# Kernel optimization log

Hardware: AMD Instinct MI355X
Metric: run time of the kernel (lower is better)

Reference implementation:

```python
import jax, jax.numpy as jnp
import numpy as np

B, N, E = 32, 1024, 16384
IN_DIM, HID, OUT = 768, 512, 400
H, F = 2, 200          # gat heads, per-head dim (H*F == OUT)
PAIR = 2 * OUT         # 800
NEG_SLOPE = 0.2


def setup_inputs() -> dict:
    key = jax.random.key(0)
    ks = jax.random.split(key, 20)
    g = lambda k, shp, fan: jax.random.normal(k, shp, jnp.float32) * (1.0 / np.sqrt(fan))
    return {
        "patch_features": jax.random.normal(ks[0], (B, N, IN_DIM), jnp.float32),
        "edges": jax.random.randint(ks[1], (2, E), 0, N, jnp.int32),
        # patch_encoder Mlps: 768 -> 512 (GELU) -> 400
        "enc_w1": g(ks[2], (IN_DIM, HID), IN_DIM), "enc_b1": jnp.zeros((HID,), jnp.float32),
        "enc_w2": g(ks[3], (HID, OUT), HID),      "enc_b2": jnp.zeros((OUT,), jnp.float32),
        # single GATConv: 400 -> 2 heads x 200, concat
        "gat_w": g(ks[4], (OUT, H, F), OUT),
        "att_src": g(ks[5], (H, F), F), "att_dst": g(ks[6], (H, F), F),
        "gat_b": jnp.zeros((H * F,), jnp.float32),
        # predict_head Mlps: 800 -> 800 (GELU) -> 400 (GELU) -> 3
        "h_w1": g(ks[7], (PAIR, PAIR), PAIR),      "h_b1": jnp.zeros((PAIR,), jnp.float32),
        "h_w2": g(ks[8], (PAIR, PAIR // 2), PAIR), "h_b2": jnp.zeros((PAIR // 2,), jnp.float32),
        "h_w3": g(ks[9], (PAIR // 2, 3), PAIR // 2), "h_b3": jnp.zeros((3,), jnp.float32),
    }


def _forward(patch_features, edges, enc_w1, enc_b1, enc_w2, enc_b2,
             gat_w, att_src, att_dst, gat_b,
             h_w1, h_b1, h_w2, h_b2, h_w3, h_b3):
    n = patch_features.shape[1]
    # per-batch patch encoder MLP (dropout inactive at eval)
    enc = jax.nn.gelu(jnp.einsum('bni,ih->bnh', patch_features, enc_w1) + enc_b1)
    enc = jnp.einsum('bnh,ho->bno', enc, enc_w2) + enc_b2   # [B,N,400]

    src0, dst0 = edges[0], edges[1]
    # GATConv adds self-loops
    loops = jnp.arange(n, dtype=edges.dtype)
    src = jnp.concatenate([src0, loops])
    dst = jnp.concatenate([dst0, loops])

    def gat(h):                                   # h: [N,400]
        wh = jnp.einsum('no,ohf->nhf', h, gat_w)  # [N,H,F]
        a_s = jnp.sum(wh * att_src, -1)           # [N,H]
        a_d = jnp.sum(wh * att_dst, -1)
        e = a_s[src] + a_d[dst]                   # [Et,H]
        e = jnp.where(e > 0, e, NEG_SLOPE * e)    # LeakyReLU(0.2)
        m = jax.ops.segment_max(e, dst, num_segments=n)
        ee = jnp.exp(e - m[dst])
        z = jax.ops.segment_sum(ee, dst, num_segments=n)
        coef = ee / z[dst]                        # softmax over incoming edges
        out = jax.ops.segment_sum(coef[:, :, None] * wh[src], dst, num_segments=n)
        return out.reshape(n, H * F) + gat_b      # concat heads + bias

    feat = enc + jax.vmap(gat)(enc)               # residual add per batch

    # pairwise edge gather + predict head
    pair = jnp.concatenate([feat[:, src0], feat[:, dst0]], axis=-1)  # [B,E,800]
    p = jax.nn.gelu(jnp.einsum('bep,pq->beq', pair, h_w1) + h_b1)
    p = jax.nn.gelu(jnp.einsum('beq,qr->ber', p, h_w2) + h_b2)
    pred = jnp.einsum('ber,rs->bes', p, h_w3) + h_b3                 # [B,E,3]
    return feat, pred


def reference(patch_features, edges, enc_w1, enc_b1, enc_w2, enc_b2,
              gat_w, att_src, att_dst, gat_b,
              h_w1, h_b1, h_w2, h_b2, h_w3, h_b3):
    return _forward(patch_features, edges, enc_w1, enc_b1, enc_w2, enc_b2,
                    gat_w, att_src, att_dst, gat_b,
                    h_w1, h_b1, h_w2, h_b2, h_w3, h_b3)
```

## Files before the change

kernel.cpp:

```cpp
#include <hip/hip_runtime.h>
#include <hip/hip_bf16.h>

typedef unsigned short u16;
typedef __attribute__((ext_vector_type(8))) short bf16x8;
typedef __attribute__((ext_vector_type(4))) float f32x4;

#define B_   32
#define N_   1024
#define E_   16384
#define ET_  17408
#define IN_DIM 768
#define HID  512
#define OUT_ 400
#define PAIR_ 800
#define UVW_ 1600
#define FEAT_ELEMS 13107200
#define MAXD 128

__device__ __forceinline__ float u2f(u16 u) {
    union { unsigned int i; float f; } v; v.i = ((unsigned int)u) << 16; return v.f;
}
__device__ __forceinline__ u16 f2u(float f) {
    __hip_bfloat16 h = __float2bfloat16(f);
    return *(u16*)&h;
}
__device__ __forceinline__ unsigned int pack2(float a, float b) {
    return (unsigned int)f2u(a) | ((unsigned int)f2u(b) << 16);
}

__device__ __forceinline__ float gelu_f(float x) {
    const float c = 0.7978845608028654f;
    float u = c * (x + 0.044715f * x * x * x);
    float t = 2.0f / (1.0f + __expf(-2.0f * u)) - 1.0f;
    return 0.5f * x * (1.0f + t);
}

__device__ __forceinline__ void load_lds16(const void* g, void* l) {
    __builtin_amdgcn_global_load_lds(
        (const __attribute__((address_space(1))) void*)g,
        (__attribute__((address_space(3))) void*)l, 16, 0, 0);
}

__global__ void wt_k(const float* __restrict__ W, u16* __restrict__ Wt,
                     int K, int N)
{
    int i = blockIdx.x * 256 + threadIdx.x;
    if (i >= N * K) return;
    int n = i / K, k = i - n * K;
    Wt[i] = f2u(W[(size_t)k * N + n]);
}

__global__ void wtuv_k(const float* __restrict__ W, u16* __restrict__ Wt)
{
    int i = blockIdx.x * 256 + threadIdx.x;
    if (i >= UVW_ * OUT_) return;
    int n = i / OUT_, k = i - n * OUT_;
    int row = (n >= PAIR_) ? OUT_ + k : k;
    int col = (n >= PAIR_) ? n - PAIR_ : n;
    Wt[i] = f2u(W[(size_t)row * PAIR_ + col]);
}

__global__ void f2b_k(const float* __restrict__ X, u16* __restrict__ Y, int n8)
{
    int i = blockIdx.x * 256 + threadIdx.x;
    if (i >= n8) return;
    const float4* p = (const float4*)X + (size_t)i * 2;
    float4 a = p[0], b = p[1];
    uint4 o;
    o.x = pack2(a.x, a.y); o.y = pack2(a.z, a.w);
    o.z = pack2(b.x, b.y); o.w = pack2(b.z, b.w);
    ((uint4*)Y)[i] = o;
}

template<int ASRC, bool DO_GELU, bool HAS_BIAS, bool OUT_F32, bool FUSE_H3, bool WIDE>
__global__ __launch_bounds__(WIDE ? 512 : 256, 2)
void mfma_gemm_k(const float* __restrict__ Af, const u16* __restrict__ Ab,
                 const u16* __restrict__ Wt, const float* __restrict__ bias,
                 u16* __restrict__ Cb, float* __restrict__ Cf,
                 int M, int N, int K,
                 const u16* __restrict__ zbuf,
                 const float* __restrict__ w3p, float* __restrict__ partp)
{
    static_assert(!WIDE || ASRC == 1, "wide path requires bf16 async staging");
    constexpr int BM  = WIDE ? 256 : 128;
    constexpr int BN  = WIDE ? 256 : 128;
    constexpr int NWV = WIDE ? 8 : 4;
    constexpr int UN  = WIDE ? 8 : 4;
    constexpr int WNS = WIDE ? 128 : 64;

    __shared__ __align__(16) u16 As[2][BM * 64];
    __shared__ __align__(16) u16 Bs[2][BN * 64];
    const int tid  = threadIdx.x;
    const int gx   = gridDim.x;
    const int nwg  = gx * gridDim.y;
    const int orig = blockIdx.y * gx + blockIdx.x;
    const int qc   = nwg >> 3, rc = nwg & 7;
    const int xcd  = orig & 7, lid = orig >> 3;
    const int wg   = ((xcd < rc) ? xcd * (qc + 1) : rc * (qc + 1) + (xcd - rc) * qc) + lid;
    const int bnIdx= wg % gx;
    const int bm   = (wg / gx) * BM;
    const int bn   = bnIdx * BN;
    const int wave = tid >> 6;
    const int lane = tid & 63;
    const int wm   = (wave >> 1) * 64;
    const int wn   = (wave & 1) * WNS;
    const int lm   = lane & 15;
    const int lq   = lane >> 4;
    const int lb   = lm & 7;
    const int l8 = lane >> 3;
    const int cl = (lane & 7) ^ l8;

    size_t arow[4]; size_t brow[4]; bool bok[4];
    #pragma unroll
    for (int c4 = 0; c4 < 4; ++c4) {
        int rt = wave * 32 + c4 * 8 + l8;
        if (ASRC == 1) arow[c4] = (size_t)(bm + rt) * K;
        int n = bn + rt;
        bok[c4] = (n < N);
        brow[c4] = (size_t)(n < N ? n : 0) * K;
    }
    const int vrow = tid >> 1, vhalf = tid & 1;

    f32x4 acc[4][UN] = {};
    const int NT = (K + 63) >> 6;

    if (ASRC == 1) {
        auto stage = [&](int buf, int k0) {
            int kk = k0 + cl * 8;
            #pragma unroll
            for (int c4 = 0; c4 < 4; ++c4) {
                const u16* ga = (kk < K) ? Ab + arow[c4] + kk : zbuf;
                load_lds16(ga, (char*)As[buf] + (wave * 32 + c4 * 8) * 128);
            }
            #pragma unroll
            for (int c4 = 0; c4 < 4; ++c4) {
                const u16* gb = (bok[c4] && kk < K) ? Wt + brow[c4] + kk : zbuf;
                load_lds16(gb, (char*)Bs[buf] + (wave * 32 + c4 * 8) * 128);
            }
        };
        stage(0, 0);
        int cur = 0;
        for (int it = 0; it < NT; ++it) {
            const bool last = (it == NT - 1);
            if (!last) stage(cur ^ 1, (it + 1) * 64);
            if (!last) asm volatile("s_waitcnt vmcnt(8)" ::: "memory");
            else       asm volatile("s_waitcnt vmcnt(0)" ::: "memory");
            __builtin_amdgcn_s_barrier();
            const char* Abase = (const char*)As[cur];
            const char* Bbase = (const char*)Bs[cur];
            #pragma unroll
            for (int kh = 0; kh < 2; ++kh) {
                bf16x8 af[4], bfr[UN];
                #pragma unroll
                for (int t = 0; t < 4; ++t)
                    af[t] = *(const bf16x8*)(Abase +
                            (wm + t * 16 + lm) * 128 + (((kh * 4 + lq) ^ lb) * 16));
                #pragma unroll
                for (int u = 0; u < UN; ++u)
                    bfr[u] = *(const bf16x8*)(Bbase +
                            (wn + u * 16 + lm) * 128 + (((kh * 4 + lq) ^ lb) * 16));
                #pragma unroll
                for (int t = 0; t < 4; ++t)
                    #pragma unroll
                    for (int u = 0; u < UN; ++u)
                        acc[t][u] = __builtin_amdgcn_mfma_f32_16x16x32_bf16(
                            af[t], bfr[u], acc[t][u], 0, 0, 0);
            }
            asm volatile("" ::: "memory");
            __builtin_amdgcn_s_barrier();
            cur ^= 1;
        }
    } else {
        for (int k0 = 0; k0 < K; k0 += 64) {
            #pragma unroll
            for (int c = 0; c < 4; ++c) {
                int c_log = vhalf * 4 + c;
                int kk = k0 + c_log * 8;
                uint4 wv = make_uint4(0, 0, 0, 0);
                if (kk < K) {
                    const float* p = Af + (size_t)(bm + vrow) * K + kk;
                    float4 v0 = *(const float4*)p;
                    float4 v1 = *(const float4*)(p + 4);
                    wv.x = pack2(v0.x, v0.y); wv.y = pack2(v0.z, v0.w);
                    wv.z = pack2(v1.x, v1.y); wv.w = pack2(v1.z, v1.w);
                }
                int pc = c_log ^ (vrow & 7);
                *(uint4*)((char*)As[0] + vrow * 128 + pc * 16) = wv;
            }
            {
                int kk = k0 + cl * 8;
                #pragma unroll
                for (int c4 = 0; c4 < 4; ++c4) {
                    const u16* gb = (bok[c4] && kk < K) ? Wt + brow[c4] + kk : zbuf;
                    load_lds16(gb, (char*)Bs[0] + (wave * 32 + c4 * 8) * 128);
                }
            }
            __syncthreads();
            #pragma unroll
            for (int kh = 0; kh < 2; ++kh) {
                bf16x8 af[4], bfr[UN];
                #pragma unroll
                for (int t = 0; t < 4; ++t)
                    af[t] = *(const bf16x8*)((const char*)As[0] +
                            (wm + t * 16 + lm) * 128 + (((kh * 4 + lq) ^ lb) * 16));
                #pragma unroll
                for (int u = 0; u < UN; ++u)
                    bfr[u] = *(const bf16x8*)((const char*)Bs[0] +
                            (wn + u * 16 + lm) * 128 + (((kh * 4 + lq) ^ lb) * 16));
                #pragma unroll
                for (int t = 0; t < 4; ++t)
                    #pragma unroll
                    for (int u = 0; u < UN; ++u)
                        acc[t][u] = __builtin_amdgcn_mfma_f32_16x16x32_bf16(
                            af[t], bfr[u], acc[t][u], 0, 0, 0);
            }
            __syncthreads();
        }
    }

    if (FUSE_H3) {
        float w3c[UN][3]; float bvv[UN];
        #pragma unroll
        for (int u = 0; u < UN; ++u) {
            int col = bn + wn + u * 16 + lm;
            bool ok = (col < N);
            bvv[u]    = ok ? bias[col] : 0.f;
            w3c[u][0] = ok ? w3p[col * 3 + 0] : 0.f;
            w3c[u][1] = ok ? w3p[col * 3 + 1] : 0.f;
            w3c[u][2] = ok ? w3p[col * 3 + 2] : 0.f;
        }
        float* red = (float*)As;
        #pragma unroll
        for (int t = 0; t < 4; ++t) {
            #pragma unroll
            for (int r = 0; r < 4; ++r) {
                float s0 = 0.f, s1 = 0.f, s2 = 0.f;
                #pragma unroll
                for (int u = 0; u < UN; ++u) {
                    float v = gelu_f(acc[t][u][r] + bvv[u]);
                    s0 += v * w3c[u][0];
                    s1 += v * w3c[u][1];
                    s2 += v * w3c[u][2];
                }
                #pragma unroll
                for (int off = 8; off; off >>= 1) {
                    s0 += __shfl_xor(s0, off);
                    s1 += __shfl_xor(s1, off);
                    s2 += __shfl_xor(s2, off);
                }
                if (lm == 0) {
                    int lr = t * 16 + lq * 4 + r;
                    float* d = red + (wave * 64 + lr) * 3;
                    d[0] = s0; d[1] = s1; d[2] = s2;
                }
            }
        }
        __syncthreads();
        if ((wave & 1) == 0) {
            int lr = lane;
            int rowg = bm + wm + lr;
            float* a = red + ((wave + 0) * 64 + lr) * 3;
            float* b = red + ((wave + 1) * 64 + lr) * 3;
            float* d = partp + ((size_t)bnIdx * M + rowg) * 3;
            d[0] = a[0] + b[0];
            d[1] = a[1] + b[1];
            d[2] = a[2] + b[2];
        }
        return;
    }

    #pragma unroll
    for (int u = 0; u < UN; ++u) {
        int col = bn + wn + u * 16 + lm;
        if (col >= N) continue;
        float bv = HAS_BIAS ? bias[col] : 0.f;
        #pragma unroll
        for (int t = 0; t < 4; ++t) {
            #pragma unroll
            for (int r = 0; r < 4; ++r) {
                int rowg = bm + wm + t * 16 + lq * 4 + r;
                float v = acc[t][u][r] + bv;
                if (DO_GELU) v = gelu_f(v);
                if (OUT_F32) {
                    Cf[(size_t)rowg * N + col] = v;
                    if (Cb) Cb[(size_t)rowg * N + col] = f2u(v);
                } else {
                    Cb[(size_t)rowg * N + col] = f2u(v);
                }
            }
        }
    }
}

__global__ __launch_bounds__(256)
void red3_k(const float* __restrict__ part, const float* __restrict__ b3,
            float* __restrict__ out, int row_base, int Mr, int ns)
{
    int r = blockIdx.x * 256 + threadIdx.x;
    if (r >= Mr) return;
    float s0 = b3[0], s1 = b3[1], s2 = b3[2];
    for (int s = 0; s < ns; ++s) {
        const float* p = part + ((size_t)s * Mr + r) * 3;
        s0 += p[0]; s1 += p[1]; s2 += p[2];
    }
    float* d = out + (size_t)FEAT_ELEMS + (size_t)(row_base + r) * 3;
    d[0] = s0; d[1] = s1; d[2] = s2;
}

__global__ __launch_bounds__(256)
void pair_fuse_k(const u16* __restrict__ UV, const float* __restrict__ b1,
                 const int* __restrict__ src0, const int* __restrict__ dst0,
                 u16* __restrict__ p1, int b0, int nrows)
{
    unsigned idx = blockIdx.x * 256u + threadIdx.x;
    unsigned total = (unsigned)nrows * 100u;
    if (idx >= total) return;
    unsigned r  = (unsigned)(((unsigned long long)idx * 1374389535ull) >> 37);
    unsigned c8 = idx - r * 100u;
    int e = r & (E_ - 1);
    int gs, gd;
    if (b0 >= 0) {
        int b = b0 + (int)(r >> 14);
        gs = (b << 10) + src0[e];
        gd = (b << 10) + dst0[e];
    } else {
        gs = src0[e]; gd = dst0[e];
    }
    uint4 qu = *(const uint4*)(UV + (size_t)gs * UVW_ + c8 * 8);
    uint4 qv = *(const uint4*)(UV + (size_t)gd * UVW_ + PAIR_ + c8 * 8);
    float4 bva = *(const float4*)(b1 + c8 * 8);
    float4 bvb = *(const float4*)(b1 + c8 * 8 + 4);
    float bb[8] = {bva.x, bva.y, bva.z, bva.w, bvb.x, bvb.y, bvb.z, bvb.w};
    unsigned int uu[4] = {qu.x, qu.y, qu.z, qu.w};
    unsigned int vv[4] = {qv.x, qv.y, qv.z, qv.w};
    uint4 o; unsigned int* op = (unsigned int*)&o;
    #pragma unroll
    for (int q = 0; q < 4; ++q) {
        float a0 = u2f((u16)(uu[q] & 0xffff)) + u2f((u16)(vv[q] & 0xffff)) + bb[2*q];
        float a1 = u2f((u16)(uu[q] >> 16))    + u2f((u16)(vv[q] >> 16))    + bb[2*q+1];
        op[q] = pack2(gelu_f(a0), gelu_f(a1));
    }
    *(uint4*)(p1 + (size_t)r * PAIR_ + c8 * 8) = o;
}

__global__ __launch_bounds__(256)
void scores_k(const u16* __restrict__ wh, const float* __restrict__ att_s,
              const float* __restrict__ att_d, float* __restrict__ a_s,
              float* __restrict__ a_d)
{
    int n = blockIdx.x * 4 + (threadIdx.x >> 6);
    int lane = threadIdx.x & 63;
    const u16* row = wh + (size_t)n * OUT_;
    float as0 = 0, as1 = 0, ad0 = 0, ad1 = 0;
    for (int f = lane; f < OUT_; f += 64) {
        float v = u2f(row[f]);
        float s = att_s[f];
        float d = att_d[f];
        if (f < 200) { as0 += v * s; ad0 += v * d; }
        else         { as1 += v * s; ad1 += v * d; }
    }
    for (int off = 32; off; off >>= 1) {
        as0 += __shfl_xor(as0, off); as1 += __shfl_xor(as1, off);
        ad0 += __shfl_xor(ad0, off); ad1 += __shfl_xor(ad1, off);
    }
    if (lane == 0) {
        a_s[(size_t)n * 2 + 0] = as0; a_s[(size_t)n * 2 + 1] = as1;
        a_d[(size_t)n * 2 + 0] = ad0; a_d[(size_t)n * 2 + 1] = ad1;
    }
}

__global__ void csr_count_k(const int* __restrict__ edges, int* __restrict__ deg)
{
    int et = blockIdx.x * blockDim.x + threadIdx.x;
    if (et >= ET_) return;
    int dst = (et < E_) ? edges[E_ + et] : (et - E_);
    atomicAdd(&deg[dst], 1);
}

__global__ __launch_bounds__(1024)
void csr_scan_k(const int* __restrict__ deg, int* __restrict__ row_ptr,
                int* __restrict__ cnt)
{
    __shared__ int s[1024];
    int t = threadIdx.x;
    int d = deg[t];
    s[t] = d;
    __syncthreads();
    for (int off = 1; off < 1024; off <<= 1) {
        int v = (t >= off) ? s[t - off] : 0;
        __syncthreads();
        s[t] += v;
        __syncthreads();
    }
    row_ptr[t] = s[t] - d;
    cnt[t] = s[t] - d;
    if (t == 1023) row_ptr[1024] = s[t];
}

__global__ void csr_fill_k(const int* __restrict__ edges, int* __restrict__ cnt,
                           int* __restrict__ col_src)
{
    int et = blockIdx.x * blockDim.x + threadIdx.x;
    if (et >= ET_) return;
    int src, dst;
    if (et < E_) { src = edges[et]; dst = edges[E_ + et]; }
    else         { src = et - E_;  dst = src; }
    int pos = atomicAdd(&cnt[dst], 1);
    col_src[pos] = src;
}

__global__ __launch_bounds__(256)
void gat_k(const u16* __restrict__ wh,
           const float* __restrict__ a_s, const float* __restrict__ a_d,
           const int* __restrict__ row_ptr, const int* __restrict__ col_src,
           const float* __restrict__ gat_b, float* __restrict__ feat,
           u16* __restrict__ featb16)
{
    int gn = blockIdx.x;
    int b = gn >> 10, n = gn & 1023;
    int tid = threadIdx.x;
    __shared__ float s_ee[2][MAXD];
    __shared__ int   s_src[MAXD];
    __shared__ float s_misc[6];
    __shared__ float s_part[4][50][9];
    int start = row_ptr[n];
    int deg = row_ptr[n + 1] - start;

    if (tid < 64) {
        int lane = tid;
        float ad0 = a_d[(size_t)gn * 2 + 0];
        float ad1 = a_d[(size_t)gn * 2 + 1];
        float m0 = -1e30f, m1 = -1e30f;
        for (int j = lane; j < deg; j += 64) {
            int gs = (b << 10) + col_src[start + j];
            float e0 = a_s[(size_t)gs * 2 + 0] + ad0; e0 = (e0 > 0.f) ? e0 : 0.2f * e0;
            float e1 = a_s[(size_t)gs * 2 + 1] + ad1; e1 = (e1 > 0.f) ? e1 : 0.2f * e1;
            if (j < MAXD) { s_ee[0][j] = e0; s_ee[1][j] = e1; s_src[j] = gs; }
            m0 = fmaxf(m0, e0); m1 = fmaxf(m1, e1);
        }
        for (int off = 32; off; off >>= 1) {
            m0 = fmaxf(m0, __shfl_xor(m0, off));
            m1 = fmaxf(m1, __shfl_xor(m1, off));
        }
        float z0 = 0.f, z1 = 0.f;
        for (int j = lane; j < deg; j += 64) {
            float e0, e1;
            if (j < MAXD) { e0 = s_ee[0][j]; e1 = s_ee[1][j]; }
            else {
                int gs = (b << 10) + col_src[start + j];
                e0 = a_s[(size_t)gs * 2 + 0] + ad0; e0 = (e0 > 0.f) ? e0 : 0.2f * e0;
                e1 = a_s[(size_t)gs * 2 + 1] + ad1; e1 = (e1 > 0.f) ? e1 : 0.2f * e1;
            }
            float t0 = __expf(e0 - m0), t1 = __expf(e1 - m1);
            if (j < MAXD) { s_ee[0][j] = t0; s_ee[1][j] = t1; }
            z0 += t0; z1 += t1;
        }
        for (int off = 32; off; off >>= 1) {
            z0 += __shfl_xor(z0, off);
            z1 += __shfl_xor(z1, off);
        }
        if (lane == 0) {
            s_misc[0] = m0; s_misc[1] = m1;
            s_misc[2] = (z0 > 0.f) ? 1.f / z0 : 0.f;
            s_misc[3] = (z1 > 0.f) ? 1.f / z1 : 0.f;
            s_misc[4] = ad0; s_misc[5] = ad1;
        }
    }
    __syncthreads();

    int wv = tid >> 6, ln = tid & 63;
    if (ln < 50) {
        int h = (ln >= 25);
        float m = s_misc[h], ad = s_misc[4 + h];
        float acc[8] = {};
        for (int j = wv; j < deg; j += 4) {
            float w; int gs;
            if (j < MAXD) { w = s_ee[h][j]; gs = s_src[j]; }
            else {
                gs = (b << 10) + col_src[start + j];
                float e = a_s[(size_t)gs * 2 + h] + ad;
                e = (e > 0.f) ? e : 0.2f * e;
                w = __expf(e - m);
            }
            uint4 q = *(const uint4*)(wh + (size_t)gs * OUT_ + ln * 8);
            acc[0] += w * u2f((u16)(q.x & 0xffff));
            acc[1] += w * u2f((u16)(q.x >> 16));
            acc[2] += w * u2f((u16)(q.y & 0xffff));
            acc[3] += w * u2f((u16)(q.y >> 16));
            acc[4] += w * u2f((u16)(q.z & 0xffff));
            acc[5] += w * u2f((u16)(q.z >> 16));
            acc[6] += w * u2f((u16)(q.w & 0xffff));
            acc[7] += w * u2f((u16)(q.w >> 16));
        }
        #pragma unroll
        for (int k = 0; k < 8; ++k) s_part[wv][ln][k] = acc[k];
    }
    __syncthreads();
    if (tid < 50) {
        int h = (tid >= 25);
        float iz = s_misc[2 + h];
        size_t base = (size_t)gn * OUT_ + tid * 8;
        float4 f0 = *(const float4*)(feat + base);
        float4 f1 = *(const float4*)(feat + base + 4);
        float fv[8] = { f0.x, f0.y, f0.z, f0.w, f1.x, f1.y, f1.z, f1.w };
        float o[8];
        #pragma unroll
        for (int k = 0; k < 8; ++k) {
            float s = s_part[0][tid][k] + s_part[1][tid][k] +
                      s_part[2][tid][k] + s_part[3][tid][k];
            o[k] = fv[k] + s * iz + gat_b[tid * 8 + k];
        }
        *(float4*)(feat + base)     = make_float4(o[0], o[1], o[2], o[3]);
        *(float4*)(feat + base + 4) = make_float4(o[4], o[5], o[6], o[7]);
        if (featb16) {
            uint4 bq;
            bq.x = pack2(o[0], o[1]); bq.y = pack2(o[2], o[3]);
            bq.z = pack2(o[4], o[5]); bq.w = pack2(o[6], o[7]);
            *(uint4*)(featb16 + base) = bq;
        }
    }
}

__global__ __launch_bounds__(256)
void head3_k(const u16* __restrict__ p2, const float* __restrict__ w3,
             const float* __restrict__ b3, float* __restrict__ out,
             int row_base, int nrows)
{
    int wv = threadIdx.x >> 6, lane = threadIdx.x & 63;
    float w3r[24];
    if (lane < 50) {
        #pragma unroll
        for (int q = 0; q < 6; ++q) {
            float4 v = *(const float4*)(w3 + lane * 24 + q * 4);
            w3r[q * 4 + 0] = v.x; w3r[q * 4 + 1] = v.y;
            w3r[q * 4 + 2] = v.z; w3r[q * 4 + 3] = v.w;
        }
    }
    int e0 = blockIdx.x * 16 + wv * 4;
    for (int ei = 0; ei < 4; ++ei) {
        int e = e0 + ei;
        if (e >= nrows) break;
        float s0 = 0, s1 = 0, s2 = 0;
        if (lane < 50) {
            uint4 q = *(const uint4*)(p2 + (size_t)e * OUT_ + lane * 8);
            float f[8];
            f[0] = u2f((u16)(q.x & 0xffff)); f[1] = u2f((u16)(q.x >> 16));
            f[2] = u2f((u16)(q.y & 0xffff)); f[3] = u2f((u16)(q.y >> 16));
            f[4] = u2f((u16)(q.z & 0xffff)); f[5] = u2f((u16)(q.z >> 16));
            f[6] = u2f((u16)(q.w & 0xffff)); f[7] = u2f((u16)(q.w >> 16));
            #pragma unroll
            for (int k = 0; k < 8; ++k) {
                s0 += f[k] * w3r[k * 3 + 0];
                s1 += f[k] * w3r[k * 3 + 1];
                s2 += f[k] * w3r[k * 3 + 2];
            }
        }
        for (int off = 32; off; off >>= 1) {
            s0 += __shfl_xor(s0, off);
            s1 += __shfl_xor(s1, off);
            s2 += __shfl_xor(s2, off);
        }
        if (lane == 0) {
            size_t o = (size_t)FEAT_ELEMS + (size_t)(row_base + e) * 3;
            out[o + 0] = s0 + b3[0];
            out[o + 1] = s1 + b3[1];
            out[o + 2] = s2 + b3[2];
        }
    }
}

extern "C" void kernel_launch(void* const* d_in, const int* in_sizes, int n_in,
                              void* d_out, int out_size, void* d_ws, size_t ws_size,
                              hipStream_t stream)
{
    const float* patch  = (const float*)d_in[0];
    const int*   edges  = (const int*)d_in[1];
    const float* enc_w1 = (const float*)d_in[2];
    const float* enc_b1 = (const float*)d_in[3];
    const float* enc_w2 = (const float*)d_in[4];
    const float* enc_b2 = (const float*)d_in[5];
    const float* gat_w  = (const float*)d_in[6];
    const float* att_s  = (const float*)d_in[7];
    const float* att_d  = (const float*)d_in[8];
    const float* gat_b  = (const float*)d_in[9];
    const float* h_w1   = (const float*)d_in[10];
    const float* h_b1   = (const float*)d_in[11];
    const float* h_w2   = (const float*)d_in[12];
    const float* h_b2   = (const float*)d_in[13];
    const float* h_w3   = (const float*)d_in[14];
    const float* h_b3   = (const float*)d_in[15];
    float* out  = (float*)d_out;
    float* feat = out;
    char*  ws   = (char*)d_ws;

    const int* src0 = edges;
    const int* dst0 = edges + E_;

    const size_t R0 = 33554432ull, TAIL = 4194304ull;
    const size_t UVSZ = 104857600ull;
    const size_t P1SZ = 26214400ull;
    int CB = 0;
    if      (ws_size >= R0 + UVSZ + TAIL + 4 * P1SZ) CB = 4;
    else if (ws_size >= R0 + UVSZ + TAIL + 2 * P1SZ) CB = 2;
    const bool big = (CB >= 2);

    u16 *enc1, *whb, *p1, *p2, *featb16, *uv, *w1t, *w2t, *gwt, *uvwt, *hw2t;
    u16 *patchb16, *encb16;
    float *a_s, *a_d, *part; int *deg;
    if (big) {
        enc1    = (u16*)ws;
        featb16 = (u16*)ws;
        part    = (float*)ws;
        whb     = (u16*)(ws + R0);
        uv      = (u16*)(ws + R0);
        encb16  = (u16*)(ws + R0 + 26214400ull);
        p1      = (u16*)(ws + R0 + UVSZ);
        patchb16= (u16*)(ws + R0 + UVSZ);
        p2      = nullptr;
        size_t tb = (ws_size - TAIL) & ~(size_t)255;
        w1t  = (u16*)(ws + tb);
        w2t  = (u16*)(ws + tb + 786432);
        gwt  = (u16*)(ws + tb + 1196032);
        uvwt = (u16*)(ws + tb + 1516032);
        hw2t = (u16*)(ws + tb + 2796032);
        a_s  = (float*)(ws + tb + 3436032);
        a_d  = (float*)(ws + tb + 3698176);
        deg  = (int*)(ws + tb + 3960320);
    } else {
        enc1    = (u16*)ws;
        whb     = (u16*)ws;
        p1      = (u16*)ws;
        featb16 = nullptr;
        patchb16= nullptr;
        encb16  = nullptr;
        part    = nullptr;
        p2      = (u16*)(ws + 26214400);
        uv      = (u16*)(ws + 39321600);
        w1t  = (u16*)(ws + 42598400);
        w2t  = (u16*)(ws + 43384832);
        gwt  = (u16*)(ws + 43794432);
        uvwt = (u16*)(ws + 44114432);
        hw2t = (u16*)(ws + 45394432);
        a_s  = (float*)(ws + 46034432);
        a_d  = (float*)(ws + 46296576);
        deg  = (int*)(ws + 46558720);
    }
    int* row_ptr = deg + 1024;
    int* cnt     = row_ptr + 1032;
    int* col_src = cnt + 1024;
    u16* zbuf = (u16*)(col_src + 17408);

    hipMemsetAsync(zbuf, 0, 256, stream);

    wt_k<<<(HID * IN_DIM + 255) / 256, 256, 0, stream>>>(enc_w1, w1t, IN_DIM, HID);
    wt_k<<<(OUT_ * HID + 255) / 256, 256, 0, stream>>>(enc_w2, w2t, HID, OUT_);
    wt_k<<<(OUT_ * OUT_ + 255) / 256, 256, 0, stream>>>(gat_w, gwt, OUT_, OUT_);
    wtuv_k<<<(UVW_ * OUT_ + 255) / 256, 256, 0, stream>>>(h_w1, uvwt);
    wt_k<<<(OUT_ * PAIR_ + 255) / 256, 256, 0, stream>>>(h_w2, hw2t, PAIR_, OUT_);

    hipMemsetAsync(deg, 0, 1024 * sizeof(int), stream);
    csr_count_k<<<(ET_ + 255) / 256, 256, 0, stream>>>(edges, deg);
    csr_scan_k<<<1, 1024, 0, stream>>>(deg, row_ptr, cnt);
    csr_fill_k<<<(ET_ + 255) / 256, 256, 0, stream>>>(edges, cnt, col_src);

    if (big) {
        f2b_k<<<(B_ * N_ * IN_DIM / 8 + 255) / 256, 256, 0, stream>>>(
            patch, patchb16, B_ * N_ * IN_DIM / 8);
        mfma_gemm_k<1, true, true, false, false, true><<<dim3(2, (B_ * N_) / 256), 512, 0, stream>>>(
            nullptr, patchb16, w1t, enc_b1, enc1, nullptr, B_ * N_, HID, IN_DIM, zbuf,
            nullptr, nullptr);
        mfma_gemm_k<1, false, true, true, false, true><<<dim3(2, (B_ * N_) / 256), 512, 0, stream>>>(
            nullptr, enc1, w2t, enc_b2, encb16, feat, B_ * N_, OUT_, HID, zbuf,
            nullptr, nullptr);
        mfma_gemm_k<1, false, false, false, false, true><<<dim3(2, (B_ * N_) / 256), 512, 0, stream>>>(
            nullptr, encb16, gwt, nullptr, whb, nullptr, B_ * N_, OUT_, OUT_, zbuf,
            nullptr, nullptr);
    } else {
        mfma_gemm_k<0, true, true, false, false, false><<<dim3(HID / 128, (B_ * N_) / 128), 256, 0, stream>>>(
            patch, nullptr, w1t, enc_b1, enc1, nullptr, B_ * N_, HID, IN_DIM, zbuf,
            nullptr, nullptr);
        mfma_gemm_k<1, false, true, true, false, false><<<dim3((OUT_ + 127) / 128, (B_ * N_) / 128), 256, 0, stream>>>(
            nullptr, enc1, w2t, enc_b2, nullptr, feat, B_ * N_, OUT_, HID, zbuf,
            nullptr, nullptr);
        mfma_gemm_k<0, false, false, false, false, false><<<dim3((OUT_ + 127) / 128, (B_ * N_) / 128), 256, 0, stream>>>(
            feat, nullptr, gwt, nullptr, whb, nullptr, B_ * N_, OUT_, OUT_, zbuf,
            nullptr, nullptr);
    }

    scores_k<<<(B_ * N_) / 4, 256, 0, stream>>>(whb, att_s, att_d, a_s, a_d);
    gat_k<<<B_ * N_, 256, 0, stream>>>(whb, a_s, a_d, row_ptr, col_src,
                                       gat_b, feat, featb16);

    if (big) {
        mfma_gemm_k<1, false, false, false, false, true><<<dim3((UVW_ + 255) / 256, (B_ * N_) / 256), 512, 0, stream>>>(
            nullptr, featb16, uvwt, nullptr, uv, nullptr, B_ * N_, UVW_, OUT_, zbuf,
            nullptr, nullptr);
        for (int b0 = 0; b0 < B_; b0 += CB) {
            int Mr = CB * E_;
            pair_fuse_k<<<(Mr * 100 + 255) / 256, 256, 0, stream>>>(
                uv, h_b1, src0, dst0, p1, b0, Mr);
            mfma_gemm_k<1, true, true, false, true, true><<<dim3((OUT_ + 255) / 256, Mr / 256), 512, 0, stream>>>(
                nullptr, p1, hw2t, h_b2, nullptr, nullptr, Mr, OUT_, PAIR_, zbuf,
                h_w3, part);
            red3_k<<<(Mr + 255) / 256, 256, 0, stream>>>(part, h_b3, out, b0 * E_, Mr,
                                                         (OUT_ + 255) / 256);
        }
    } else {
        for (int b = 0; b < B_; ++b) {
            const float* featb = feat + (size_t)b * N_ * OUT_;
            mfma_gemm_k<0, false, false, false, false, false><<<dim3((UVW_ + 127) / 128, N_ / 128), 256, 0, stream>>>(
                featb, nullptr, uvwt, nullptr, uv, nullptr, N_, UVW_, OUT_, zbuf,
                nullptr, nullptr);
            pair_fuse_k<<<(E_ * 100 + 255) / 256, 256, 0, stream>>>(
                uv, h_b1, src0, dst0, p1, -1, E_);
            mfma_gemm_k<1, true, true, false, false, false><<<dim3((OUT_ + 127) / 128, E_ / 128), 256, 0, stream>>>(
                nullptr, p1, hw2t, h_b2, p2, nullptr, E_, OUT_, PAIR_, zbuf,
                nullptr, nullptr);
            head3_k<<<(E_ + 15) / 16, 256, 0, stream>>>(p2, h_w3, h_b3, out,
                                                        b * E_, E_);
        }
    }
}
```

Measured before the change: 1.502 ms.

## Add 128x512 GEMM tile shape for predict-head layer 2 to cover full N

Adds a third tile shape (BM=128, BN=512, BK=32, 8 waves in a 2x4 layout) to the MFMA GEMM. It is used for the fused h_w2+h_w3 predict-head GEMM so one block covers all 400 output columns. Previously N=400 was split across two 256-wide blocks, which padded the second block heavily and made the A tile load twice. The partial-sum buffer and the red3 reduction now handle a single column block. The trade-offs are a shorter K step, which means more barriers per tile, a different LDS swizzle, and 112 of the 512 columns still padded.

```diff
diff --git a/kernel.cpp b/kernel.cpp
--- a/kernel.cpp
+++ b/kernel.cpp
@@ -72,8 +72,8 @@
     ((uint4*)Y)[i] = o;
 }
 
-template<int ASRC, bool DO_GELU, bool HAS_BIAS, bool OUT_F32, bool FUSE_H3, bool WIDE>
-__global__ __launch_bounds__(WIDE ? 512 : 256, 2)
+template<int ASRC, bool DO_GELU, bool HAS_BIAS, bool OUT_F32, bool FUSE_H3, int SHAPE>
+__global__ __launch_bounds__(SHAPE >= 1 ? 512 : 256, 2)
 void mfma_gemm_k(const float* __restrict__ Af, const u16* __restrict__ Ab,
                  const u16* __restrict__ Wt, const float* __restrict__ bias,
                  u16* __restrict__ Cb, float* __restrict__ Cf,
@@ -81,15 +81,17 @@
                  const u16* __restrict__ zbuf,
                  const float* __restrict__ w3p, float* __restrict__ partp)
 {
-    static_assert(!WIDE || ASRC == 1, "wide path requires bf16 async staging");
-    constexpr int BM  = WIDE ? 256 : 128;
-    constexpr int BN  = WIDE ? 256 : 128;
-    constexpr int NWV = WIDE ? 8 : 4;
-    constexpr int UN  = WIDE ? 8 : 4;
-    constexpr int WNS = WIDE ? 128 : 64;
-
-    __shared__ __align__(16) u16 As[2][BM * 64];
-    __shared__ __align__(16) u16 Bs[2][BN * 64];
+    static_assert(SHAPE == 0 || ASRC == 1, "wide shapes require bf16 async staging");
+    constexpr int BM  = (SHAPE == 2) ? 128 : (SHAPE == 1 ? 256 : 128);
+    constexpr int BN  = (SHAPE == 2) ? 512 : (SHAPE == 1 ? 256 : 128);
+    constexpr int NWV = (SHAPE >= 1) ? 8 : 4;
+    constexpr int UN  = (SHAPE >= 1) ? 8 : 4;
+    constexpr int BKT = (SHAPE == 2) ? 32 : 64;
+    constexpr int KH  = (SHAPE == 2) ? 1 : 2;
+    constexpr int CW  = (SHAPE == 2) ? 4 : 2;
+
+    __shared__ __align__(16) u16 As[2][BM * BKT];
+    __shared__ __align__(16) u16 Bs[2][BN * BKT];
     const int tid  = threadIdx.x;
     const int gx   = gridDim.x;
     const int nwg  = gx * gridDim.y;
@@ -102,63 +104,101 @@
     const int bn   = bnIdx * BN;
     const int wave = tid >> 6;
     const int lane = tid & 63;
-    const int wm   = (wave >> 1) * 64;
-    const int wn   = (wave & 1) * WNS;
+    const int wm   = (SHAPE == 2) ? (wave >> 2) * 64 : (wave >> 1) * 64;
+    const int wn   = (SHAPE == 2) ? (wave & 3) * 128
+                   : (SHAPE == 1) ? (wave & 1) * 128 : (wave & 1) * 64;
     const int lm   = lane & 15;
     const int lq   = lane >> 4;
     const int lb   = lm & 7;
     const int l8 = lane >> 3;
     const int cl = (lane & 7) ^ l8;
+    const int l4 = lane >> 2;
+    const int ck = lane & 3;
+    const int cl2 = ck ^ ((l4 >> 1) & 3);
 
     size_t arow[4]; size_t brow[4]; bool bok[4];
-    #pragma unroll
-    for (int c4 = 0; c4 < 4; ++c4) {
-        int rt = wave * 32 + c4 * 8 + l8;
-        if (ASRC == 1) arow[c4] = (size_t)(bm + rt) * K;
-        int n = bn + rt;
-        bok[c4] = (n < N);
-        brow[c4] = (size_t)(n < N ? n : 0) * K;
+    size_t arowS = 0;
+    if (SHAPE == 2) {
+        arowS = (size_t)(bm + wave * 16 + l4) * K;
+        #pragma unroll
+        for (int c4 = 0; c4 < 4; ++c4) {
+            int n = bn + wave * 64 + c4 * 16 + l4;
+            bok[c4] = (n < N);
+            brow[c4] = (size_t)(n < N ? n : 0) * K;
+        }
+    } else {
+        #pragma unroll
+        for (int c4 = 0; c4 < 4; ++c4) {
+            int rt = wave * 32 + c4 * 8 + l8;
+            if (ASRC == 1) arow[c4] = (size_t)(bm + rt) * K;
+            int n = bn + rt;
+            bok[c4] = (n < N);
+            brow[c4] = (size_t)(n < N ? n : 0) * K;
+        }
     }
     const int vrow = tid >> 1, vhalf = tid & 1;
 
     f32x4 acc[4][UN] = {};
-    const int NT = (K + 63) >> 6;
+    const int NT = (K + BKT - 1) / BKT;
 
     if (ASRC == 1) {
         auto stage = [&](int buf, int k0) {
-            int kk = k0 + cl * 8;
-            #pragma unroll
-            for (int c4 = 0; c4 < 4; ++c4) {
-                const u16* ga = (kk < K) ? Ab + arow[c4] + kk : zbuf;
-                load_lds16(ga, (char*)As[buf] + (wave * 32 + c4 * 8) * 128);
-            }
-            #pragma unroll
-            for (int c4 = 0; c4 < 4; ++c4) {
-                const u16* gb = (bok[c4] && kk < K) ? Wt + brow[c4] + kk : zbuf;
-                load_lds16(gb, (char*)Bs[buf] + (wave * 32 + c4 * 8) * 128);
+            if (SHAPE == 2) {
+                int kk = k0 + cl2 * 8;
+                const u16* ga = (kk < K) ? Ab + arowS + kk : zbuf;
+                load_lds16(ga, (char*)As[buf] + wave * 16 * 64);
+                #pragma unroll
+                for (int c4 = 0; c4 < 4; ++c4) {
+                    const u16* gb = (bok[c4] && kk < K) ? Wt + brow[c4] + kk : zbuf;
+                    load_lds16(gb, (char*)Bs[buf] + (wave * 64 + c4 * 16) * 64);
+                }
+            } else {
+                int kk = k0 + cl * 8;
+                #pragma unroll
+                for (int c4 = 0; c4 < 4; ++c4) {
+                    const u16* ga = (kk < K) ? Ab + arow[c4] + kk : zbuf;
+                    load_lds16(ga, (char*)As[buf] + (wave * 32 + c4 * 8) * 128);
+                }
+                #pragma unroll
+                for (int c4 = 0; c4 < 4; ++c4) {
+                    const u16* gb = (bok[c4] && kk < K) ? Wt + brow[c4] + kk : zbuf;
+                    load_lds16(gb, (char*)Bs[buf] + (wave * 32 + c4 * 8) * 128);
+                }
             }
         };
         stage(0, 0);
         int cur = 0;
         for (int it = 0; it < NT; ++it) {
             const bool last = (it == NT - 1);
-            if (!last) stage(cur ^ 1, (it + 1) * 64);
-            if (!last) asm volatile("s_waitcnt vmcnt(8)" ::: "memory");
-            else       asm volatile("s_waitcnt vmcnt(0)" ::: "memory");
+            if (!last) stage(cur ^ 1, (it + 1) * BKT);
+            if (!last) {
+                if (SHAPE == 2) asm volatile("s_waitcnt vmcnt(5)" ::: "memory");
+                else            asm volatile("s_waitcnt vmcnt(8)" ::: "memory");
+            } else {
+                asm volatile("s_waitcnt vmcnt(0)" ::: "memory");
+            }
             __builtin_amdgcn_s_barrier();
             const char* Abase = (const char*)As[cur];
             const char* Bbase = (const char*)Bs[cur];
             #pragma unroll
-            for (int kh = 0; kh < 2; ++kh) {
+            for (int kh = 0; kh < KH; ++kh) {
                 bf16x8 af[4], bfr[UN];
                 #pragma unroll
-                for (int t = 0; t < 4; ++t)
-                    af[t] = *(const bf16x8*)(Abase +
-                            (wm + t * 16 + lm) * 128 + (((kh * 4 + lq) ^ lb) * 16));
-                #pragma unroll
-                for (int u = 0; u < UN; ++u)
-                    bfr[u] = *(const bf16x8*)(Bbase +
-                            (wn + u * 16 + lm) * 128 + (((kh * 4 + lq) ^ lb) * 16));
+                for (int t = 0; t < 4; ++t) {
+                    int row = wm + t * 16 + lm;
+                    int off = (SHAPE == 2)
+                        ? row * 64 + ((lq ^ ((row >> 1) & 3)) * 16)
+                        : row * 128 + (((kh * 4 + lq) ^ lb) * 16);
+                    af[t] = *(const bf16x8*)(Abase + off);
+                }
+                #pragma unroll
+                for (int u = 0; u < UN; ++u) {
+                    int row = wn + u * 16 + lm;
+                    int off = (SHAPE == 2)
+                        ? row * 64 + ((lq ^ ((row >> 1) & 3)) * 16)
+                        : row * 128 + (((kh * 4 + lq) ^ lb) * 16);
+                    bfr[u] = *(const bf16x8*)(Bbase + off);
+                }
                 #pragma unroll
                 for (int t = 0; t < 4; ++t)
                     #pragma unroll
@@ -256,15 +296,17 @@
             }
         }
         __syncthreads();
-        if ((wave & 1) == 0) {
+        if ((wave & (CW - 1)) == 0) {
             int lr = lane;
             int rowg = bm + wm + lr;
-            float* a = red + ((wave + 0) * 64 + lr) * 3;
-            float* b = red + ((wave + 1) * 64 + lr) * 3;
+            float s0 = 0.f, s1 = 0.f, s2 = 0.f;
+            #pragma unroll
+            for (int w = 0; w < CW; ++w) {
+                float* a = red + ((wave + w) * 64 + lr) * 3;
+                s0 += a[0]; s1 += a[1]; s2 += a[2];
+            }
             float* d = partp + ((size_t)bnIdx * M + rowg) * 3;
-            d[0] = a[0] + b[0];
-            d[1] = a[1] + b[1];
-            d[2] = a[2] + b[2];
+            d[0] = s0; d[1] = s1; d[2] = s2;
         }
         return;
     }
@@ -666,23 +708,23 @@
     if (big) {
         f2b_k<<<(B_ * N_ * IN_DIM / 8 + 255) / 256, 256, 0, stream>>>(
             patch, patchb16, B_ * N_ * IN_DIM / 8);
-        mfma_gemm_k<1, true, true, false, false, true><<<dim3(2, (B_ * N_) / 256), 512, 0, stream>>>(
+        mfma_gemm_k<1, true, true, false, false, 1><<<dim3(2, (B_ * N_) / 256), 512, 0, stream>>>(
             nullptr, patchb16, w1t, enc_b1, enc1, nullptr, B_ * N_, HID, IN_DIM, zbuf,
             nullptr, nullptr);
-        mfma_gemm_k<1, false, true, true, false, true><<<dim3(2, (B_ * N_) / 256), 512, 0, stream>>>(
+        mfma_gemm_k<1, false, true, true, false, 1><<<dim3(2, (B_ * N_) / 256), 512, 0, stream>>>(
             nullptr, enc1, w2t, enc_b2, encb16, feat, B_ * N_, OUT_, HID, zbuf,
             nullptr, nullptr);
-        mfma_gemm_k<1, false, false, false, false, true><<<dim3(2, (B_ * N_) / 256), 512, 0, stream>>>(
+        mfma_gemm_k<1, false, false, false, false, 1><<<dim3(2, (B_ * N_) / 256), 512, 0, stream>>>(
             nullptr, encb16, gwt, nullptr, whb, nullptr, B_ * N_, OUT_, OUT_, zbuf,
             nullptr, nullptr);
     } else {
-        mfma_gemm_k<0, true, true, false, false, false><<<dim3(HID / 128, (B_ * N_) / 128), 256, 0, stream>>>(
+        mfma_gemm_k<0, true, true, false, false, 0><<<dim3(HID / 128, (B_ * N_) / 128), 256, 0, stream>>>(
             patch, nullptr, w1t, enc_b1, enc1, nullptr, B_ * N_, HID, IN_DIM, zbuf,
             nullptr, nullptr);
-        mfma_gemm_k<1, false, true, true, false, false><<<dim3((OUT_ + 127) / 128, (B_ * N_) / 128), 256, 0, stream>>>(
+        mfma_gemm_k<1, false, true, true, false, 0><<<dim3((OUT_ + 127) / 128, (B_ * N_) / 128), 256, 0, stream>>>(
             nullptr, enc1, w2t, enc_b2, nullptr, feat, B_ * N_, OUT_, HID, zbuf,
             nullptr, nullptr);
-        mfma_gemm_k<0, false, false, false, false, false><<<dim3((OUT_ + 127) / 128, (B_ * N_) / 128), 256, 0, stream>>>(
+        mfma_gemm_k<0, false, false, false, false, 0><<<dim3((OUT_ + 127) / 128, (B_ * N_) / 128), 256, 0, stream>>>(
             feat, nullptr, gwt, nullptr, whb, nullptr, B_ * N_, OUT_, OUT_, zbuf,
             nullptr, nullptr);
     }
@@ -692,28 +734,27 @@
                                        gat_b, feat, featb16);
 
     if (big) {
-        mfma_gemm_k<1, false, false, false, false, true><<<dim3((UVW_ + 255) / 256, (B_ * N_) / 256), 512, 0, stream>>>(
+        mfma_gemm_k<1, false, false, false, false, 1><<<dim3((UVW_ + 255) / 256, (B_ * N_) / 256), 512, 0, stream>>>(
             nullptr, featb16, uvwt, nullptr, uv, nullptr, B_ * N_, UVW_, OUT_, zbuf,
             nullptr, nullptr);
         for (int b0 = 0; b0 < B_; b0 += CB) {
             int Mr = CB * E_;
             pair_fuse_k<<<(Mr * 100 + 255) / 256, 256, 0, stream>>>(
                 uv, h_b1, src0, dst0, p1, b0, Mr);
-            mfma_gemm_k<1, true, true, false, true, true><<<dim3((OUT_ + 255) / 256, Mr / 256), 512, 0, stream>>>(
+            mfma_gemm_k<1, true, true, false, true, 2><<<dim3(1, Mr / 128), 512, 0, stream>>>(
                 nullptr, p1, hw2t, h_b2, nullptr, nullptr, Mr, OUT_, PAIR_, zbuf,
                 h_w3, part);
-            red3_k<<<(Mr + 255) / 256, 256, 0, stream>>>(part, h_b3, out, b0 * E_, Mr,
-                                                         (OUT_ + 255) / 256);
+            red3_k<<<(Mr + 255) / 256, 256, 0, stream>>>(part, h_b3, out, b0 * E_, Mr, 1);
         }
     } else {
         for (int b = 0; b < B_; ++b) {
             const float* featb = feat + (size_t)b * N_ * OUT_;
-            mfma_gemm_k<0, false, false, false, false, false><<<dim3((UVW_ + 127) / 128, N_ / 128), 256, 0, stream>>>(
+            mfma_gemm_k<0, false, false, false, false, 0><<<dim3((UVW_ + 127) / 128, N_ / 128), 256, 0, stream>>>(
                 featb, nullptr, uvwt, nullptr, uv, nullptr, N_, UVW_, OUT_, zbuf,
                 nullptr, nullptr);
             pair_fuse_k<<<(E_ * 100 + 255) / 256, 256, 0, stream>>>(
                 uv, h_b1, src0, dst0, p1, -1, E_);
-            mfma_gemm_k<1, true, true, false, false, false><<<dim3((OUT_ + 127) / 128, E_ / 128), 256, 0, stream>>>(
+            mfma_gemm_k<1, true, true, false, false, 0><<<dim3((OUT_ + 127) / 128, E_ / 128), 256, 0, stream>>>(
                 nullptr, p1, hw2t, h_b2, p2, nullptr, E_, OUT_, PAIR_, zbuf,
                 nullptr, nullptr);
             head3_k<<<(E_ + 15) / 16, 256, 0, stream>>>(p2, h_w3, h_b3, out,
```

Result: slower. 1.641 ms (+9.2%).

## Fuse pair gather, bias and GELU into head GEMM A-tile staging

Applied to the files above, without the earlier changes.

The separate pair_fuse kernel and its p1 intermediate go away. The second head GEMM now gathers the u and v rows by src/dst edge index directly during A-tile staging, adds h_b1, applies GELU and writes the bf16 tile to LDS. This removes the write and reread of the large p1 buffer and the per-chunk launch loop, so all batches run in one launch. In exchange the A operand uses synchronous register loads plus ALU work inside the pipelined loop instead of async LDS loads, which may weaken load/compute overlap, and the GELU is recomputed for each of the two N-tiles.

```diff
diff --git a/kernel.cpp b/kernel.cpp
--- a/kernel.cpp
+++ b/kernel.cpp
@@ -72,21 +72,22 @@
     ((uint4*)Y)[i] = o;
 }
 
-template<int ASRC, bool DO_GELU, bool HAS_BIAS, bool OUT_F32, bool FUSE_H3, bool WIDE>
-__global__ __launch_bounds__(WIDE ? 512 : 256, 2)
+template<int ASRC, bool DO_GELU, bool HAS_BIAS, bool OUT_F32, bool FUSE_H3, int SHAPE>
+__global__ __launch_bounds__(SHAPE >= 1 ? 512 : 256, 2)
 void mfma_gemm_k(const float* __restrict__ Af, const u16* __restrict__ Ab,
                  const u16* __restrict__ Wt, const float* __restrict__ bias,
                  u16* __restrict__ Cb, float* __restrict__ Cf,
                  int M, int N, int K,
                  const u16* __restrict__ zbuf,
-                 const float* __restrict__ w3p, float* __restrict__ partp)
-{
-    static_assert(!WIDE || ASRC == 1, "wide path requires bf16 async staging");
-    constexpr int BM  = WIDE ? 256 : 128;
-    constexpr int BN  = WIDE ? 256 : 128;
-    constexpr int NWV = WIDE ? 8 : 4;
-    constexpr int UN  = WIDE ? 8 : 4;
-    constexpr int WNS = WIDE ? 128 : 64;
+                 const float* __restrict__ w3p, float* __restrict__ partp,
+                 const int* __restrict__ src0p, const int* __restrict__ dst0p,
+                 int b0)
+{
+    static_assert(SHAPE == 0 || ASRC >= 1, "wide shapes need bf16/gather staging");
+    constexpr int BM  = (SHAPE == 1) ? 256 : 128;
+    constexpr int BN  = (SHAPE == 1) ? 256 : 128;
+    constexpr int UN  = (SHAPE == 1) ? 8 : 4;
+    constexpr int CW  = 2;
 
     __shared__ __align__(16) u16 As[2][BM * 64];
     __shared__ __align__(16) u16 Bs[2][BN * 64];
@@ -103,7 +104,7 @@
     const int wave = tid >> 6;
     const int lane = tid & 63;
     const int wm   = (wave >> 1) * 64;
-    const int wn   = (wave & 1) * WNS;
+    const int wn   = (SHAPE == 1) ? (wave & 1) * 128 : (wave & 1) * 64;
     const int lm   = lane & 15;
     const int lq   = lane >> 4;
     const int lb   = lm & 7;
@@ -119,23 +120,77 @@
         bok[c4] = (n < N);
         brow[c4] = (size_t)(n < N ? n : 0) * K;
     }
+    int gsv[4], gdv[4];
+    if (ASRC == 2) {
+        #pragma unroll
+        for (int c = 0; c < 4; ++c) {
+            int gr = bm + wave * 32 + c * 8 + (lane >> 3);
+            int e  = gr & (E_ - 1);
+            int b  = b0 + (gr >> 14);
+            gsv[c] = (b << 10) + src0p[e];
+            gdv[c] = (b << 10) + dst0p[e];
+        }
+    }
     const int vrow = tid >> 1, vhalf = tid & 1;
 
     f32x4 acc[4][UN] = {};
     const int NT = (K + 63) >> 6;
 
-    if (ASRC == 1) {
+    if (ASRC >= 1) {
         auto stage = [&](int buf, int k0) {
-            int kk = k0 + cl * 8;
-            #pragma unroll
-            for (int c4 = 0; c4 < 4; ++c4) {
-                const u16* ga = (kk < K) ? Ab + arow[c4] + kk : zbuf;
-                load_lds16(ga, (char*)As[buf] + (wave * 32 + c4 * 8) * 128);
-            }
-            #pragma unroll
-            for (int c4 = 0; c4 < 4; ++c4) {
-                const u16* gb = (bok[c4] && kk < K) ? Wt + brow[c4] + kk : zbuf;
-                load_lds16(gb, (char*)Bs[buf] + (wave * 32 + c4 * 8) * 128);
+            if (ASRC == 2) {
+                int kk  = k0 + (lane & 7) * 8;
+                int kkb = k0 + cl * 8;
+                bool okk = (kk < PAIR_);
+                uint4 qu[4], qv[4];
+                float4 bA = make_float4(0, 0, 0, 0), bB = bA;
+                if (okk) {
+                    bA = *(const float4*)(Af + kk);
+                    bB = *(const float4*)(Af + kk + 4);
+                    #pragma unroll
+                    for (int c = 0; c < 4; ++c) {
+                        qu[c] = *(const uint4*)(Ab + (size_t)gsv[c] * UVW_ + kk);
+                        qv[c] = *(const uint4*)(Ab + (size_t)gdv[c] * UVW_ + PAIR_ + kk);
+                    }
+                }
+                #pragma unroll
+                for (int c4 = 0; c4 < 4; ++c4) {
+                    const u16* gb = (bok[c4] && kkb < K) ? Wt + brow[c4] + kkb : zbuf;
+                    load_lds16(gb, (char*)Bs[buf] + (wave * 32 + c4 * 8) * 128);
+                }
+                float bb[8] = {bA.x, bA.y, bA.z, bA.w, bB.x, bB.y, bB.z, bB.w};
+                #pragma unroll
+                for (int c = 0; c < 4; ++c) {
+                    int r = wave * 32 + c * 8 + (lane >> 3);
+                    uint4 wv = make_uint4(0, 0, 0, 0);
+                    if (okk) {
+                        unsigned uu[4] = {qu[c].x, qu[c].y, qu[c].z, qu[c].w};
+                        unsigned vv[4] = {qv[c].x, qv[c].y, qv[c].z, qv[c].w};
+                        unsigned* op = (unsigned*)&wv;
+                        #pragma unroll
+                        for (int q = 0; q < 4; ++q) {
+                            float a0 = u2f((u16)(uu[q] & 0xffff)) +
+                                       u2f((u16)(vv[q] & 0xffff)) + bb[2 * q];
+                            float a1 = u2f((u16)(uu[q] >> 16)) +
+                                       u2f((u16)(vv[q] >> 16)) + bb[2 * q + 1];
+                            op[q] = pack2(gelu_f(a0), gelu_f(a1));
+                        }
+                    }
+                    int pc = (lane & 7) ^ (r & 7);
+                    *(uint4*)((char*)As[buf] + r * 128 + pc * 16) = wv;
+                }
+            } else {
+                int kk = k0 + cl * 8;
+                #pragma unroll
+                for (int c4 = 0; c4 < 4; ++c4) {
+                    const u16* ga = (kk < K) ? Ab + arow[c4] + kk : zbuf;
+                    load_lds16(ga, (char*)As[buf] + (wave * 32 + c4 * 8) * 128);
+                }
+                #pragma unroll
+                for (int c4 = 0; c4 < 4; ++c4) {
+                    const u16* gb = (bok[c4] && kk < K) ? Wt + brow[c4] + kk : zbuf;
+                    load_lds16(gb, (char*)Bs[buf] + (wave * 32 + c4 * 8) * 128);
+                }
             }
         };
         stage(0, 0);
@@ -143,8 +198,12 @@
         for (int it = 0; it < NT; ++it) {
             const bool last = (it == NT - 1);
             if (!last) stage(cur ^ 1, (it + 1) * 64);
-            if (!last) asm volatile("s_waitcnt vmcnt(8)" ::: "memory");
-            else       asm volatile("s_waitcnt vmcnt(0)" ::: "memory");
+            if (!last) {
+                if (ASRC == 2) asm volatile("s_waitcnt vmcnt(4) lgkmcnt(0)" ::: "memory");
+                else           asm volatile("s_waitcnt vmcnt(8)" ::: "memory");
+            } else {
+                asm volatile("s_waitcnt vmcnt(0) lgkmcnt(0)" ::: "memory");
+            }
             __builtin_amdgcn_s_barrier();
             const char* Abase = (const char*)As[cur];
             const char* Bbase = (const char*)Bs[cur];
@@ -256,15 +315,17 @@
             }
         }
         __syncthreads();
-        if ((wave & 1) == 0) {
+        if ((wave & (CW - 1)) == 0) {
             int lr = lane;
             int rowg = bm + wm + lr;
-            float* a = red + ((wave + 0) * 64 + lr) * 3;
-            float* b = red + ((wave + 1) * 64 + lr) * 3;
+            float s0 = 0.f, s1 = 0.f, s2 = 0.f;
+            #pragma unroll
+            for (int w = 0; w < CW; ++w) {
+                float* a = red + ((wave + w) * 64 + lr) * 3;
+                s0 += a[0]; s1 += a[1]; s2 += a[2];
+            }
             float* d = partp + ((size_t)bnIdx * M + rowg) * 3;
-            d[0] = a[0] + b[0];
-            d[1] = a[1] + b[1];
-            d[2] = a[2] + b[2];
+            d[0] = s0; d[1] = s1; d[2] = s2;
         }
         return;
     }
@@ -599,10 +660,7 @@
     const size_t R0 = 33554432ull, TAIL = 4194304ull;
     const size_t UVSZ = 104857600ull;
     const size_t P1SZ = 26214400ull;
-    int CB = 0;
-    if      (ws_size >= R0 + UVSZ + TAIL + 4 * P1SZ) CB = 4;
-    else if (ws_size >= R0 + UVSZ + TAIL + 2 * P1SZ) CB = 2;
-    const bool big = (CB >= 2);
+    const bool big = (ws_size >= R0 + UVSZ + TAIL + 2 * P1SZ);
 
     u16 *enc1, *whb, *p1, *p2, *featb16, *uv, *w1t, *w2t, *gwt, *uvwt, *hw2t;
     u16 *patchb16, *encb16;
@@ -614,8 +672,8 @@
         whb     = (u16*)(ws + R0);
         uv      = (u16*)(ws + R0);
         encb16  = (u16*)(ws + R0 + 26214400ull);
-        p1      = (u16*)(ws + R0 + UVSZ);
         patchb16= (u16*)(ws + R0 + UVSZ);
+        p1      = nullptr;
         p2      = nullptr;
         size_t tb = (ws_size - TAIL) & ~(size_t)255;
         w1t  = (u16*)(ws + tb);
@@ -666,25 +724,25 @@
     if (big) {
         f2b_k<<<(B_ * N_ * IN_DIM / 8 + 255) / 256, 256, 0, stream>>>(
             patch, patchb16, B_ * N_ * IN_DIM / 8);
-        mfma_gemm_k<1, true, true, false, false, true><<<dim3(2, (B_ * N_) / 256), 512, 0, stream>>>(
+        mfma_gemm_k<1, true, true, false, false, 1><<<dim3(2, (B_ * N_) / 256), 512, 0, stream>>>(
             nullptr, patchb16, w1t, enc_b1, enc1, nullptr, B_ * N_, HID, IN_DIM, zbuf,
-            nullptr, nullptr);
-        mfma_gemm_k<1, false, true, true, false, true><<<dim3(2, (B_ * N_) / 256), 512, 0, stream>>>(
+            nullptr, nullptr, nullptr, nullptr, 0);
+        mfma_gemm_k<1, false, true, true, false, 1><<<dim3(2, (B_ * N_) / 256), 512, 0, stream>>>(
             nullptr, enc1, w2t, enc_b2, encb16, feat, B_ * N_, OUT_, HID, zbuf,
-            nullptr, nullptr);
-        mfma_gemm_k<1, false, false, false, false, true><<<dim3(2, (B_ * N_) / 256), 512, 0, stream>>>(
+            nullptr, nullptr, nullptr, nullptr, 0);
+        mfma_gemm_k<1, false, false, false, false, 1><<<dim3(2, (B_ * N_) / 256), 512, 0, stream>>>(
             nullptr, encb16, gwt, nullptr, whb, nullptr, B_ * N_, OUT_, OUT_, zbuf,
-            nullptr, nullptr);
+            nullptr, nullptr, nullptr, nullptr, 0);
     } else {
-        mfma_gemm_k<0, true, true, false, false, false><<<dim3(HID / 128, (B_ * N_) / 128), 256, 0, stream>>>(
+        mfma_gemm_k<0, true, true, false, false, 0><<<dim3(HID / 128, (B_ * N_) / 128), 256, 0, stream>>>(
             patch, nullptr, w1t, enc_b1, enc1, nullptr, B_ * N_, HID, IN_DIM, zbuf,
-            nullptr, nullptr);
-        mfma_gemm_k<1, false, true, true, false, false><<<dim3((OUT_ + 127) / 128, (B_ * N_) / 128), 256, 0, stream>>>(
+            nullptr, nullptr, nullptr, nullptr, 0);
+        mfma_gemm_k<1, false, true, true, false, 0><<<dim3((OUT_ + 127) / 128, (B_ * N_) / 128), 256, 0, stream>>>(
             nullptr, enc1, w2t, enc_b2, nullptr, feat, B_ * N_, OUT_, HID, zbuf,
-            nullptr, nullptr);
-        mfma_gemm_k<0, false, false, false, false, false><<<dim3((OUT_ + 127) / 128, (B_ * N_) / 128), 256, 0, stream>>>(
+            nullptr, nullptr, nullptr, nullptr, 0);
+        mfma_gemm_k<0, false, false, false, false, 0><<<dim3((OUT_ + 127) / 128, (B_ * N_) / 128), 256, 0, stream>>>(
             feat, nullptr, gwt, nullptr, whb, nullptr, B_ * N_, OUT_, OUT_, zbuf,
-            nullptr, nullptr);
+            nullptr, nullptr, nullptr, nullptr, 0);
     }
 
     scores_k<<<(B_ * N_) / 4, 256, 0, stream>>>(whb, att_s, att_d, a_s, a_d);
@@ -692,30 +750,25 @@
                                        gat_b, feat, featb16);
 
     if (big) {
-        mfma_gemm_k<1, false, false, false, false, true><<<dim3((UVW_ + 255) / 256, (B_ * N_) / 256), 512, 0, stream>>>(
+        mfma_gemm_k<1, false, false, false, false, 1><<<dim3((UVW_ + 255) / 256, (B_ * N_) / 256), 512, 0, stream>>>(
             nullptr, featb16, uvwt, nullptr, uv, nullptr, B_ * N_, UVW_, OUT_, zbuf,
-            nullptr, nullptr);
-        for (int b0 = 0; b0 < B_; b0 += CB) {
-            int Mr = CB * E_;
-            pair_fuse_k<<<(Mr * 100 + 255) / 256, 256, 0, stream>>>(
-                uv, h_b1, src0, dst0, p1, b0, Mr);
-            mfma_gemm_k<1, true, true, false, true, true><<<dim3((OUT_ + 255) / 256, Mr / 256), 512, 0, stream>>>(
-                nullptr, p1, hw2t, h_b2, nullptr, nullptr, Mr, OUT_, PAIR_, zbuf,
-                h_w3, part);
-            red3_k<<<(Mr + 255) / 256, 256, 0, stream>>>(part, h_b3, out, b0 * E_, Mr,
-                                                         (OUT_ + 255) / 256);
-        }
+            nullptr, nullptr, nullptr, nullptr, 0);
+        const int Mr = B_ * E_;
+        mfma_gemm_k<2, false, true, false, true, 1><<<dim3(2, Mr / 256), 512, 0, stream>>>(
+            h_b1 , uv , hw2t, h_b2, nullptr, nullptr,
+            Mr, OUT_, PAIR_, zbuf, h_w3, part, src0, dst0, 0);
+        red3_k<<<(Mr + 255) / 256, 256, 0, stream>>>(part, h_b3, out, 0, Mr, 2);
     } else {
         for (int b = 0; b < B_; ++b) {
             const float* featb = feat + (size_t)b * N_ * OUT_;
-            mfma_gemm_k<0, false, false, false, false, false><<<dim3((UVW_ + 127) / 128, N_ / 128), 256, 0, stream>>>(
+            mfma_gemm_k<0, false, false, false, false, 0><<<dim3((UVW_ + 127) / 128, N_ / 128), 256, 0, stream>>>(
                 featb, nullptr, uvwt, nullptr, uv, nullptr, N_, UVW_, OUT_, zbuf,
-                nullptr, nullptr);
+                nullptr, nullptr, nullptr, nullptr, 0);
             pair_fuse_k<<<(E_ * 100 + 255) / 256, 256, 0, stream>>>(
                 uv, h_b1, src0, dst0, p1, -1, E_);
-            mfma_gemm_k<1, true, true, false, false, false><<<dim3((OUT_ + 127) / 128, E_ / 128), 256, 0, stream>>>(
+            mfma_gemm_k<1, true, true, false, false, 0><<<dim3((OUT_ + 127) / 128, E_ / 128), 256, 0, stream>>>(
                 nullptr, p1, hw2t, h_b2, p2, nullptr, E_, OUT_, PAIR_, zbuf,
-                nullptr, nullptr);
+                nullptr, nullptr, nullptr, nullptr, 0);
             head3_k<<<(E_ + 15) / 16, 256, 0, stream>>>(p2, h_w3, h_b3, out,
                                                         b * E_, E_);
         }
```

Measured after the change: 1.810 ms. +20.5%, slower.
